# Optimization experiments

Hardware: AMD Instinct MI355X
Metric: run time of the kernel (lower is better)

## Reference

```python
import jax, jax.numpy as jnp
import numpy as np

EPS = 1e-6

def _rmsnorm(x, w):
    # normalize over last (head_dim) axis
    return x * jax.lax.rsqrt(jnp.mean(x * x, axis=-1, keepdims=True) + EPS) * w

def _rope(x, cos, sin):
    # x: [B, H, S, D]; cos/sin: [S, D]
    d = x.shape[-1]
    x1, x2 = x[..., : d // 2], x[..., d // 2 :]
    rot = jnp.concatenate([-x2, x1], axis=-1)
    return x * cos[None, None] + rot * sin[None, None]

def setup_inputs() -> dict:
    key = jax.random.key(0)
    B, S, D_MODEL = 1, 2048, 2048
    HEADS, HEAD_DIM, NKV = 32, 64, 8
    d_out = HEADS * HEAD_DIM
    kv_d_out = NKV * HEAD_DIM
    ks = jax.random.split(key, 8)
    x = jax.random.normal(ks[0], (B, S, D_MODEL), dtype=jnp.float32)
    # RoPE tables
    inv_freq = 1.0 / (10000.0 ** (jnp.arange(0, HEAD_DIM, 2, dtype=jnp.float32) / HEAD_DIM))
    pos = jnp.arange(S, dtype=jnp.float32)
    ang = pos[:, None] * inv_freq[None, :]            # [S, D/2]
    ang = jnp.concatenate([ang, ang], axis=-1)        # [S, D]
    sin, cos = jnp.sin(ang), jnp.cos(ang)
    mask = jnp.tril(jnp.ones((S, S), dtype=bool))     # causal: True = attend
    sd = 0.02
    Wq = jax.random.normal(ks[1], (D_MODEL, d_out), dtype=jnp.float32) * sd
    Wk = jax.random.normal(ks[2], (D_MODEL, kv_d_out), dtype=jnp.float32) * sd
    Wv = jax.random.normal(ks[3], (D_MODEL, kv_d_out), dtype=jnp.float32) * sd
    Wo = jax.random.normal(ks[4], (d_out, D_MODEL), dtype=jnp.float32) * sd
    bo = jnp.zeros((D_MODEL,), dtype=jnp.float32)
    q_scale = jnp.ones((HEAD_DIM,), dtype=jnp.float32)
    k_scale = jnp.ones((HEAD_DIM,), dtype=jnp.float32)
    return {"x": x, "sin": sin, "cos": cos, "mask": mask, "Wq": Wq, "Wk": Wk,
            "Wv": Wv, "Wo": Wo, "bo": bo, "q_scale": q_scale, "k_scale": k_scale}

def reference(x, sin, cos, mask, Wq, Wk, Wv, Wo, bo, q_scale, k_scale):
    B, S, _ = x.shape
    HEADS, HEAD_DIM, NKV = 32, 64, 8
    GS = HEADS // NKV  # group size = 4
    q = (x @ Wq).reshape(B, S, HEADS, HEAD_DIM).transpose(0, 2, 1, 3)  # [B,H,S,D]
    k = (x @ Wk).reshape(B, S, NKV, HEAD_DIM).transpose(0, 2, 1, 3)    # [B,G,S,D]
    v = (x @ Wv).reshape(B, S, NKV, HEAD_DIM).transpose(0, 2, 1, 3)    # [B,G,S,D]
    q = _rmsnorm(q, q_scale)
    k = _rmsnorm(k, k_scale)
    q = _rope(q, cos, sin)
    k = _rope(k, cos, sin)
    # GQA without materializing repeated k/v: group query heads per kv group
    qg = q.reshape(B, NKV, GS, S, HEAD_DIM)
    scale = 1.0 / jnp.sqrt(jnp.asarray(HEAD_DIM, dtype=x.dtype))
    scores = jnp.einsum('bghqd,bgkd->bghqk', qg, k) * scale  # [B,G,Gs,S,S]
    scores = jnp.where(mask[None, None, None], scores, jnp.asarray(-jnp.inf, dtype=scores.dtype))
    attn = jax.nn.softmax(scores, axis=-1)
    out = jnp.einsum('bghqk,bgkd->bghqd', attn, v)            # [B,G,Gs,S,D]
    out = out.reshape(B, HEADS, S, HEAD_DIM).transpose(0, 2, 1, 3).reshape(B, S, HEADS * HEAD_DIM)
    return out @ Wo + bo
```

## Files before the change

kernel.cpp:

```cpp
#include <hip/hip_runtime.h>
#include <stdint.h>


typedef __bf16 bf16x8 __attribute__((ext_vector_type(8)));
typedef __bf16 bf16x4v __attribute__((ext_vector_type(4)));
typedef float f32x4 __attribute__((ext_vector_type(4)));

#define MFMA_BF16(a, b, c) __builtin_amdgcn_mfma_f32_16x16x32_bf16(a, b, c, 0, 0, 0)

#if __has_builtin(__builtin_amdgcn_exp2f)
#define EXP2F(x) __builtin_amdgcn_exp2f(x)
#else
#define EXP2F(x) __expf((x) * 0.69314718055994531f)
#endif

#define QSCALE 0.18033688011112042f
#define SHIFT2 11.541560327111707f

__device__ __forceinline__ unsigned short f2bf(float f) {
  unsigned int u = __float_as_uint(f);
  u += 0x7fffu + ((u >> 16) & 1u);
  return (unsigned short)(u >> 16);
}
__device__ __forceinline__ float bf2f(unsigned short b) {
  return __uint_as_float(((unsigned int)b) << 16);
}

__device__ __forceinline__ void gload_lds16(const unsigned short* gsrc,
                                            unsigned short* ldst) {
  __builtin_amdgcn_global_load_lds(
      (const __attribute__((address_space(1))) unsigned int*)gsrc,
      (__attribute__((address_space(3))) unsigned int*)ldst, 16, 0, 0);
}

__global__ __launch_bounds__(256) void cvt_bf16(const float* __restrict__ X,
                                                unsigned short* __restrict__ Y, int n) {
  int i = (blockIdx.x * 256 + threadIdx.x) * 4;
  if (i < n) {
    float4 v = *(const float4*)&X[i];
    ushort4 o;
    o.x = f2bf(v.x); o.y = f2bf(v.y); o.z = f2bf(v.z); o.w = f2bf(v.w);
    *(ushort4*)&Y[i] = o;
  }
}

__global__ __launch_bounds__(256) void transpose_all(const float* __restrict__ Wq,
                                                     const float* __restrict__ Wk,
                                                     const float* __restrict__ Wv,
                                                     const float* __restrict__ Wo,
                                                     unsigned short* __restrict__ Wqkvt,
                                                     unsigned short* __restrict__ Wot) {
  int bx = blockIdx.x;
  const float* W;
  unsigned short* T;
  int N, nb;
  if (bx < 32)      { W = Wq; T = Wqkvt;                       N = 2048; nb = bx * 64; }
  else if (bx < 40) { W = Wk; T = Wqkvt + 2048 * 2048;         N = 512;  nb = (bx - 32) * 64; }
  else if (bx < 48) { W = Wv; T = Wqkvt + (size_t)2560 * 2048; N = 512;  nb = (bx - 40) * 64; }
  else              { W = Wo; T = Wot;                         N = 2048; nb = (bx - 48) * 64; }
  int kb = blockIdx.y * 64;
  int tid = threadIdx.x;
  __shared__ float tile[64][65];
#pragma unroll
  for (int i = 0; i < 16; i++) {
    int idx = tid + i * 256;
    int r = idx >> 6, c = idx & 63;
    tile[r][c] = W[(size_t)(kb + r) * N + nb + c];
  }
  __syncthreads();
#pragma unroll
  for (int i = 0; i < 8; i++) {
    int idx = tid + i * 256;
    int r = idx >> 5, cp = idx & 31;
    ushort2 o;
    o.x = f2bf(tile[2 * cp][r]);
    o.y = f2bf(tile[2 * cp + 1][r]);
    *(ushort2*)&T[(size_t)(nb + r) * 2048 + kb + 2 * cp] = o;
  }
}

#define GEMM_DBUF(A_, B_, m0_, n0_)                                            \
  int quad = lane >> 4, l16 = lane & 15;                                       \
  int wrow = (w & 1) * 32, wcol = (w >> 1) * 64;                               \
  int rsub = lane >> 3, csub = lane & 7;                                       \
  int chunk = csub ^ rsub;                                                     \
  int slotL = quad ^ (l16 & 7);                                                \
  const unsigned short* gA = &A_[(size_t)(m0_ + w * 16 + rsub) * 2048 + chunk * 8]; \
  const unsigned short* gB = &B_[(size_t)(n0_ + w * 32 + rsub) * 2048 + chunk * 8]; \
  int laOff = (w * 16) * 64 + lane * 8;                                        \
  int lbOff = 64 * 64 + (w * 32) * 64 + lane * 8;                              \
  f32x4 acc[2][4];                                                             \
  _Pragma("unroll") for (int i = 0; i < 2; i++)                                \
      _Pragma("unroll") for (int j = 0; j < 4; j++)                            \
          acc[i][j] = (f32x4){0.f, 0.f, 0.f, 0.f};                             \
  {                                                                            \
    unsigned short* sp = &Stage[0][0];                                         \
    gload_lds16(gA, sp + laOff);                                               \
    gload_lds16(gA + 8 * 2048, sp + laOff + 8 * 64);                           \
    gload_lds16(gB, sp + lbOff);                                               \
    gload_lds16(gB + 8 * 2048, sp + lbOff + 8 * 64);                           \
    gload_lds16(gB + 16 * 2048, sp + lbOff + 16 * 64);                         \
    gload_lds16(gB + 24 * 2048, sp + lbOff + 24 * 64);                         \
  }                                                                            \
  for (int k0 = 0; k0 < 2048; k0 += 64) {                                      \
    __syncthreads();                                                           \
    unsigned short* cur = &Stage[(k0 >> 6) & 1][0];                            \
    unsigned short* nxt = &Stage[((k0 >> 6) + 1) & 1][0];                      \
    if (k0 + 64 < 2048) {                                                      \
      int kn = k0 + 64;                                                        \
      gload_lds16(gA + kn, nxt + laOff);                                       \
      gload_lds16(gA + 8 * 2048 + kn, nxt + laOff + 8 * 64);                   \
      gload_lds16(gB + kn, nxt + lbOff);                                       \
      gload_lds16(gB + 8 * 2048 + kn, nxt + lbOff + 8 * 64);                   \
      gload_lds16(gB + 16 * 2048 + kn, nxt + lbOff + 16 * 64);                 \
      gload_lds16(gB + 24 * 2048 + kn, nxt + lbOff + 24 * 64);                 \
    }                                                                          \
    const unsigned short* As = cur;                                            \
    const unsigned short* Bs = cur + 64 * 64;                                  \
    bf16x8 af[2][2], bfr[4][2];                                                \
    _Pragma("unroll") for (int i = 0; i < 2; i++) {                            \
      int base = (wrow + i * 16 + l16) * 64;                                   \
      af[i][0] = *(const bf16x8*)&As[base + slotL * 8];                        \
      af[i][1] = *(const bf16x8*)&As[base + (slotL ^ 4) * 8];                  \
    }                                                                          \
    _Pragma("unroll") for (int j = 0; j < 4; j++) {                            \
      int base = (wcol + j * 16 + l16) * 64;                                   \
      bfr[j][0] = *(const bf16x8*)&Bs[base + slotL * 8];                       \
      bfr[j][1] = *(const bf16x8*)&Bs[base + (slotL ^ 4) * 8];                 \
    }                                                                          \
    _Pragma("unroll") for (int kc = 0; kc < 2; kc++)                           \
        _Pragma("unroll") for (int i = 0; i < 2; i++)                          \
            _Pragma("unroll") for (int j = 0; j < 4; j++)                      \
                acc[i][j] = MFMA_BF16(af[i][kc], bfr[j][kc], acc[i][j]);       \
  }

__global__ __launch_bounds__(256, 3) void gemm_qkv(const unsigned short* __restrict__ A,
                                                   const unsigned short* __restrict__ B,
                                                   const float* __restrict__ sinp,
                                                   const float* __restrict__ cosp,
                                                   const float* __restrict__ q_scale,
                                                   const float* __restrict__ k_scale,
                                                   unsigned short* __restrict__ qh,
                                                   unsigned short* __restrict__ kh,
                                                   unsigned short* __restrict__ vtmp) {
  __shared__ __align__(16) unsigned short Stage[2][192 * 64];
  int tid = threadIdx.x;
  int w = tid >> 6, lane = tid & 63;
  int m0 = blockIdx.y * 64;
  int n0 = blockIdx.x * 128;
  GEMM_DBUF(A, B, m0, n0)

  int hd = blockIdx.x * 2 + (w >> 1);
  if (hd < 40) {
    const float* scl = (hd < 32) ? q_scale : k_scale;
    float wsc[4];
#pragma unroll
    for (int j = 0; j < 4; j++) wsc[j] = scl[j * 16 + l16];
    float oscale = (hd < 32) ? QSCALE : 1.0f;
#pragma unroll
    for (int i = 0; i < 2; i++)
#pragma unroll
      for (int r = 0; r < 4; r++) {
        float ss = 0.f;
#pragma unroll
        for (int j = 0; j < 4; j++) ss += acc[i][j][r] * acc[i][j][r];
#pragma unroll
        for (int off = 8; off; off >>= 1) ss += __shfl_xor(ss, off);
        float inv = rsqrtf(ss * (1.f / 64.f) + 1e-6f);
        int s = m0 + wrow + i * 16 + quad * 4 + r;
        float xn[4];
#pragma unroll
        for (int j = 0; j < 4; j++) xn[j] = acc[i][j][r] * inv * wsc[j];
#pragma unroll
        for (int j = 0; j < 4; j++) {
          int d = j * 16 + l16;
          float rot = (j < 2) ? -xn[j + 2] : xn[j - 2];
          float out = (xn[j] * cosp[s * 64 + d] + rot * sinp[s * 64 + d]) * oscale;
          if (hd < 32) qh[(size_t)s * 2048 + hd * 64 + d] = f2bf(out);
          else         kh[(size_t)s * 512 + (hd - 32) * 64 + d] = f2bf(out);
        }
      }
  } else {
    int g = hd - 40;
#pragma unroll
    for (int i = 0; i < 2; i++)
#pragma unroll
      for (int r = 0; r < 4; r++) {
        int s = m0 + wrow + i * 16 + quad * 4 + r;
#pragma unroll
        for (int j = 0; j < 4; j++)
          vtmp[(size_t)s * 512 + g * 64 + j * 16 + l16] = f2bf(acc[i][j][r]);
      }
  }
}

__global__ __launch_bounds__(256, 3) void gemm_out(const unsigned short* __restrict__ A,
                                                   const unsigned short* __restrict__ B,
                                                   float* __restrict__ C,
                                                   const float* __restrict__ bias) {
  __shared__ __align__(16) unsigned short Stage[2][192 * 64];
  int tid = threadIdx.x;
  int w = tid >> 6, lane = tid & 63;
  int m0 = blockIdx.y * 64;
  int n0 = blockIdx.x * 128;
  GEMM_DBUF(A, B, m0, n0)

#pragma unroll
  for (int i = 0; i < 2; i++) {
    int row = m0 + wrow + i * 16 + quad * 4;
#pragma unroll
    for (int j = 0; j < 4; j++) {
      int col = n0 + wcol + j * 16 + l16;
      float b = bias[col];
#pragma unroll
      for (int r = 0; r < 4; r++)
        C[(size_t)(row + r) * 2048 + col] = acc[i][j][r] + b;
    }
  }
}

__global__ __launch_bounds__(256) void v_transpose(const unsigned short* __restrict__ vtmp,
                                                   unsigned short* __restrict__ vt) {
  __shared__ unsigned short tile[64][65];
  int s0 = blockIdx.x * 64;
  int g = blockIdx.y;
  int tid = threadIdx.x;
#pragma unroll
  for (int i = 0; i < 16; i++) {
    int idx = tid + i * 256;
    int r = idx >> 6, c = idx & 63;
    tile[r][c] = vtmp[(size_t)(s0 + r) * 512 + g * 64 + c];
  }
  __syncthreads();
#pragma unroll
  for (int i = 0; i < 16; i++) {
    int idx = tid + i * 256;
    int d = idx >> 6, slot = idx & 63;
    int qd = (slot >> 3) & 3, c = slot >> 5, j = slot & 7;
    int key = 16 * ((j >> 2) * 2 + c) + qd * 4 + (j & 3);
    vt[(size_t)(g * 64 + d) * 2048 + s0 + slot] = tile[key][d];
  }
}

__global__ __launch_bounds__(256, 4) void attention(const unsigned short* __restrict__ qh,
                                                    const unsigned short* __restrict__ kh,
                                                    const unsigned short* __restrict__ vt,
                                                    unsigned short* __restrict__ Opart,
                                                    float* __restrict__ Lpart) {
  int h = blockIdx.y;
  int g = h >> 2;
  int z = blockIdx.z;
  int tile = (blockIdx.x + blockIdx.y) & 31;
  int q0 = tile * 64;
  int w = threadIdx.x >> 6;
  int lane = threadIdx.x & 63;
  int quad = lane >> 4;
  int l16 = lane & 15;
  int qrow0 = q0 + w * 16;

  __shared__ __align__(16) unsigned short Stage[8192];
  unsigned short* Ks = Stage;
  unsigned short* Vs = Stage + 4096;

  int rsub = lane >> 3;
  int csub = lane & 7;
  int chunk = csub ^ rsub;

  const unsigned short* kg = &kh[(size_t)(w * 16 + rsub) * 512 + g * 64 + chunk * 8];
  const unsigned short* vg = &vt[(size_t)(g * 64 + w * 16 + rsub) * 2048 + chunk * 8];
  unsigned short* kl = Ks + (w * 16) * 64 + lane * 8;
  unsigned short* vl = Vs + (w * 16) * 64 + lane * 8;

  int posL = quad ^ (l16 & 7);
  int fL = l16 * 64 + posL * 8;
  int fH = l16 * 64 + (posL ^ 4) * 8;

  bf16x8 bq0 = *(const bf16x8*)&qh[(size_t)(qrow0 + l16) * 2048 + h * 64 + quad * 8];
  bf16x8 bq1 = *(const bf16x8*)&qh[(size_t)(qrow0 + l16) * 2048 + h * 64 + 32 + quad * 8];

  f32x4 o[4];
#pragma unroll
  for (int j = 0; j < 4; j++) o[j] = (f32x4){0.f, 0.f, 0.f, 0.f};
  float l_run = 0.f;

  int T = tile + 1;
  int it0 = z ? (T >> 1) : 0;
  int it1 = z ? T : (T >> 1);
  for (int it = it0; it < it1; ++it) {
    int n0 = it << 6;
    __syncthreads();
    gload_lds16(kg + (size_t)n0 * 512, kl);
    gload_lds16(kg + (size_t)(n0 + 8) * 512, kl + 8 * 64);
    gload_lds16(vg + n0, vl);
    gload_lds16(vg + n0 + 8 * 2048, vl + 8 * 64);
    __syncthreads();

    f32x4 s[4];
#pragma unroll
    for (int t = 0; t < 4; ++t) {
      bf16x8 kfl = *(const bf16x8*)&Ks[t * 1024 + fL];
      bf16x8 kfh = *(const bf16x8*)&Ks[t * 1024 + fH];
      f32x4 zz = (f32x4){0.f, 0.f, 0.f, 0.f};
      zz = MFMA_BF16(kfl, bq0, zz);
      s[t] = MFMA_BF16(kfh, bq1, zz);
    }

    float pv[4][4];
    if (it == T - 1) {
      int qg = qrow0 + l16;
#pragma unroll
      for (int t = 0; t < 4; ++t)
#pragma unroll
        for (int r = 0; r < 4; ++r) {
          int key = n0 + t * 16 + quad * 4 + r;
          float p = (key <= qg) ? EXP2F(s[t][r] - SHIFT2) : 0.f;
          l_run += p;
          pv[t][r] = p;
        }
    } else {
#pragma unroll
      for (int t = 0; t < 4; ++t)
#pragma unroll
        for (int r = 0; r < 4; ++r) {
          float p = EXP2F(s[t][r] - SHIFT2);
          l_run += p;
          pv[t][r] = p;
        }
    }

    bf16x8 pf0, pf1;
#pragma unroll
    for (int j = 0; j < 4; ++j) {
      pf0[j] = (__bf16)pv[0][j];
      pf0[j + 4] = (__bf16)pv[2][j];
      pf1[j] = (__bf16)pv[1][j];
      pf1[j + 4] = (__bf16)pv[3][j];
    }

#pragma unroll
    for (int jd = 0; jd < 4; ++jd) {
      bf16x8 vfl = *(const bf16x8*)&Vs[jd * 1024 + fL];
      bf16x8 vfh = *(const bf16x8*)&Vs[jd * 1024 + fH];
      o[jd] = MFMA_BF16(vfl, pf0, o[jd]);
      o[jd] = MFMA_BF16(vfh, pf1, o[jd]);
    }
  }

  l_run += __shfl_xor(l_run, 16);
  l_run += __shfl_xor(l_run, 32);
  if (lane < 16)
    Lpart[(size_t)z * 65536 + (qrow0 + l16) * 32 + h] = l_run;

  __syncthreads();
  unsigned short* Ob = Stage + w * (16 * 68);
#pragma unroll
  for (int jd = 0; jd < 4; ++jd) {
    bf16x4v pk;
#pragma unroll
    for (int r = 0; r < 4; ++r) pk[r] = (__bf16)o[jd][r];
    *(bf16x4v*)&Ob[l16 * 68 + jd * 16 + quad * 4] = pk;
  }
  __threadfence_block();
#pragma unroll
  for (int rr = 0; rr < 2; ++rr) {
    int cidx = rr * 64 + lane;
    int row = cidx >> 3, ch = cidx & 7;
    bf16x8 v = *(const bf16x8*)&Ob[row * 68 + ch * 8];
    *(bf16x8*)&Opart[((size_t)z * 2048 + qrow0 + row) * 2048 + h * 64 + ch * 8] = v;
  }
}

__global__ __launch_bounds__(256) void combine(const unsigned short* __restrict__ Opart,
                                               const float* __restrict__ Lpart,
                                               unsigned short* __restrict__ aout) {
  int idx = blockIdx.x * 256 + threadIdx.x;
  int s = idx >> 9;
  int col = (idx & 511) * 4;
  int h = col >> 6;
  float l = Lpart[s * 32 + h] + Lpart[65536 + s * 32 + h];
  float linv = 1.f / l;
  ushort4 a = *(const ushort4*)&Opart[(size_t)s * 2048 + col];
  ushort4 b = *(const ushort4*)&Opart[(size_t)(2048 + s) * 2048 + col];
  ushort4 o;
  o.x = f2bf((bf2f(a.x) + bf2f(b.x)) * linv);
  o.y = f2bf((bf2f(a.y) + bf2f(b.y)) * linv);
  o.z = f2bf((bf2f(a.z) + bf2f(b.z)) * linv);
  o.w = f2bf((bf2f(a.w) + bf2f(b.w)) * linv);
  *(ushort4*)&aout[(size_t)s * 2048 + col] = o;
}

extern "C" void kernel_launch(void* const* d_in, const int* in_sizes, int n_in,
                              void* d_out, int out_size, void* d_ws, size_t ws_size,
                              hipStream_t stream) {
  (void)in_sizes; (void)n_in; (void)out_size; (void)ws_size;
  const float* x    = (const float*)d_in[0];
  const float* sinp = (const float*)d_in[1];
  const float* cosp = (const float*)d_in[2];
  const float* Wq = (const float*)d_in[4];
  const float* Wk = (const float*)d_in[5];
  const float* Wv = (const float*)d_in[6];
  const float* Wo = (const float*)d_in[7];
  const float* bo = (const float*)d_in[8];
  const float* q_scale = (const float*)d_in[9];
  const float* k_scale = (const float*)d_in[10];
  float* outp = (float*)d_out;

  uint8_t* ws = (uint8_t*)d_ws;
  const size_t MB = 1024 * 1024;
  unsigned short* xb    = (unsigned short*)(ws);
  unsigned short* Wqkvt = (unsigned short*)(ws + 8 * MB);
  unsigned short* Wot   = (unsigned short*)(ws + 20 * MB);
  unsigned short* qh    = (unsigned short*)(ws + 28 * MB);
  unsigned short* kh    = (unsigned short*)(ws + 36 * MB);
  unsigned short* vtmp  = (unsigned short*)(ws + 38 * MB);
  unsigned short* vt    = (unsigned short*)(ws + 40 * MB);
  unsigned short* aout  = (unsigned short*)(ws + 42 * MB);
  unsigned short* Opart = (unsigned short*)(ws + 50 * MB);
  float*          Lpart = (float*)(ws + 66 * MB);

  cvt_bf16<<<4096, 256, 0, stream>>>(x, xb, 2048 * 2048);
  transpose_all<<<dim3(80, 32), 256, 0, stream>>>(Wq, Wk, Wv, Wo, Wqkvt, Wot);
  gemm_qkv<<<dim3(24, 32), 256, 0, stream>>>(xb, Wqkvt, sinp, cosp, q_scale, k_scale,
                                             qh, kh, vtmp);
  v_transpose<<<dim3(32, 8), 256, 0, stream>>>(vtmp, vt);
  attention<<<dim3(32, 32, 2), 256, 0, stream>>>(qh, kh, vt, Opart, Lpart);
  combine<<<4096, 256, 0, stream>>>(Opart, Lpart, aout);
  gemm_out<<<dim3(16, 32), 256, 0, stream>>>(aout, Wot, outp, bo);
}
```

Before: 222.9 us.

## Fuse x conversion, V transpose and split-K combine into neighbouring kernels

Folds the x fp32-to-bf16 conversion into the weight-transpose launch as extra blocks, writes V straight into the permuted transposed layout from the QKV GEMM epilogue, and drops the two-way split of attention over keys along with its combine kernel. Each attention block now normalizes by 1/l itself and writes bf16 output directly. This cuts launch count and the intermediate global traffic for vtmp, Opart and Lpart. The cost is half as many attention blocks with causal-imbalanced work, so long-tail tiles lose parallelism.

```diff
diff --git a/kernel.cpp b/kernel.cpp
--- a/kernel.cpp
+++ b/kernel.cpp
@@ -22,9 +22,6 @@
   u += 0x7fffu + ((u >> 16) & 1u);
   return (unsigned short)(u >> 16);
 }
-__device__ __forceinline__ float bf2f(unsigned short b) {
-  return __uint_as_float(((unsigned int)b) << 16);
-}
 
 __device__ __forceinline__ void gload_lds16(const unsigned short* gsrc,
                                             unsigned short* ldst) {
@@ -33,24 +30,28 @@
       (__attribute__((address_space(3))) unsigned int*)ldst, 16, 0, 0);
 }
 
-__global__ __launch_bounds__(256) void cvt_bf16(const float* __restrict__ X,
-                                                unsigned short* __restrict__ Y, int n) {
-  int i = (blockIdx.x * 256 + threadIdx.x) * 4;
-  if (i < n) {
-    float4 v = *(const float4*)&X[i];
-    ushort4 o;
-    o.x = f2bf(v.x); o.y = f2bf(v.y); o.z = f2bf(v.z); o.w = f2bf(v.w);
-    *(ushort4*)&Y[i] = o;
-  }
-}
-
 __global__ __launch_bounds__(256) void transpose_all(const float* __restrict__ Wq,
                                                      const float* __restrict__ Wk,
                                                      const float* __restrict__ Wv,
                                                      const float* __restrict__ Wo,
+                                                     const float* __restrict__ x,
                                                      unsigned short* __restrict__ Wqkvt,
-                                                     unsigned short* __restrict__ Wot) {
+                                                     unsigned short* __restrict__ Wot,
+                                                     unsigned short* __restrict__ xb) {
   int bx = blockIdx.x;
+  int tid = threadIdx.x;
+  if (bx >= 80) {
+    int bid = (bx - 80) * 32 + blockIdx.y;
+#pragma unroll
+    for (int p = 0; p < 8; p++) {
+      int i = bid * 8192 + p * 1024 + tid * 4;
+      float4 v = *(const float4*)&x[i];
+      ushort4 o;
+      o.x = f2bf(v.x); o.y = f2bf(v.y); o.z = f2bf(v.z); o.w = f2bf(v.w);
+      *(ushort4*)&xb[i] = o;
+    }
+    return;
+  }
   const float* W;
   unsigned short* T;
   int N, nb;
@@ -59,7 +60,6 @@
   else if (bx < 48) { W = Wv; T = Wqkvt + (size_t)2560 * 2048; N = 512;  nb = (bx - 40) * 64; }
   else              { W = Wo; T = Wot;                         N = 2048; nb = (bx - 48) * 64; }
   int kb = blockIdx.y * 64;
-  int tid = threadIdx.x;
   __shared__ float tile[64][65];
 #pragma unroll
   for (int i = 0; i < 16; i++) {
@@ -142,7 +142,7 @@
                                                    const float* __restrict__ k_scale,
                                                    unsigned short* __restrict__ qh,
                                                    unsigned short* __restrict__ kh,
-                                                   unsigned short* __restrict__ vtmp) {
+                                                   unsigned short* __restrict__ vt) {
   __shared__ __align__(16) unsigned short Stage[2][192 * 64];
   int tid = threadIdx.x;
   int w = tid >> 6, lane = tid & 63;
@@ -183,14 +183,17 @@
   } else {
     int g = hd - 40;
 #pragma unroll
-    for (int i = 0; i < 2; i++)
-#pragma unroll
-      for (int r = 0; r < 4; r++) {
-        int s = m0 + wrow + i * 16 + quad * 4 + r;
-#pragma unroll
-        for (int j = 0; j < 4; j++)
-          vtmp[(size_t)s * 512 + g * 64 + j * 16 + l16] = f2bf(acc[i][j][r]);
+    for (int i = 0; i < 2; i++) {
+      int t = (wrow + i * 16) >> 4;
+      int slotb = (t & 1) * 32 + quad * 8 + (t >> 1) * 4;
+#pragma unroll
+      for (int j = 0; j < 4; j++) {
+        bf16x4v pk;
+#pragma unroll
+        for (int r = 0; r < 4; r++) pk[r] = (__bf16)acc[i][j][r];
+        *(bf16x4v*)&vt[(size_t)(g * 64 + j * 16 + l16) * 2048 + m0 + slotb] = pk;
       }
+    }
   }
 }
 
@@ -219,37 +222,12 @@
   }
 }
 
-__global__ __launch_bounds__(256) void v_transpose(const unsigned short* __restrict__ vtmp,
-                                                   unsigned short* __restrict__ vt) {
-  __shared__ unsigned short tile[64][65];
-  int s0 = blockIdx.x * 64;
-  int g = blockIdx.y;
-  int tid = threadIdx.x;
-#pragma unroll
-  for (int i = 0; i < 16; i++) {
-    int idx = tid + i * 256;
-    int r = idx >> 6, c = idx & 63;
-    tile[r][c] = vtmp[(size_t)(s0 + r) * 512 + g * 64 + c];
-  }
-  __syncthreads();
-#pragma unroll
-  for (int i = 0; i < 16; i++) {
-    int idx = tid + i * 256;
-    int d = idx >> 6, slot = idx & 63;
-    int qd = (slot >> 3) & 3, c = slot >> 5, j = slot & 7;
-    int key = 16 * ((j >> 2) * 2 + c) + qd * 4 + (j & 3);
-    vt[(size_t)(g * 64 + d) * 2048 + s0 + slot] = tile[key][d];
-  }
-}
-
 __global__ __launch_bounds__(256, 4) void attention(const unsigned short* __restrict__ qh,
                                                     const unsigned short* __restrict__ kh,
                                                     const unsigned short* __restrict__ vt,
-                                                    unsigned short* __restrict__ Opart,
-                                                    float* __restrict__ Lpart) {
+                                                    unsigned short* __restrict__ aout) {
   int h = blockIdx.y;
   int g = h >> 2;
-  int z = blockIdx.z;
   int tile = (blockIdx.x + blockIdx.y) & 31;
   int q0 = tile * 64;
   int w = threadIdx.x >> 6;
@@ -284,9 +262,7 @@
   float l_run = 0.f;
 
   int T = tile + 1;
-  int it0 = z ? (T >> 1) : 0;
-  int it1 = z ? T : (T >> 1);
-  for (int it = it0; it < it1; ++it) {
+  for (int it = 0; it < T; ++it) {
     int n0 = it << 6;
     __syncthreads();
     gload_lds16(kg + (size_t)n0 * 512, kl);
@@ -348,8 +324,7 @@
 
   l_run += __shfl_xor(l_run, 16);
   l_run += __shfl_xor(l_run, 32);
-  if (lane < 16)
-    Lpart[(size_t)z * 65536 + (qrow0 + l16) * 32 + h] = l_run;
+  float linv = 1.f / l_run;
 
   __syncthreads();
   unsigned short* Ob = Stage + w * (16 * 68);
@@ -357,7 +332,7 @@
   for (int jd = 0; jd < 4; ++jd) {
     bf16x4v pk;
 #pragma unroll
-    for (int r = 0; r < 4; ++r) pk[r] = (__bf16)o[jd][r];
+    for (int r = 0; r < 4; ++r) pk[r] = (__bf16)(o[jd][r] * linv);
     *(bf16x4v*)&Ob[l16 * 68 + jd * 16 + quad * 4] = pk;
   }
   __threadfence_block();
@@ -366,27 +341,8 @@
     int cidx = rr * 64 + lane;
     int row = cidx >> 3, ch = cidx & 7;
     bf16x8 v = *(const bf16x8*)&Ob[row * 68 + ch * 8];
-    *(bf16x8*)&Opart[((size_t)z * 2048 + qrow0 + row) * 2048 + h * 64 + ch * 8] = v;
-  }
-}
-
-__global__ __launch_bounds__(256) void combine(const unsigned short* __restrict__ Opart,
-                                               const float* __restrict__ Lpart,
-                                               unsigned short* __restrict__ aout) {
-  int idx = blockIdx.x * 256 + threadIdx.x;
-  int s = idx >> 9;
-  int col = (idx & 511) * 4;
-  int h = col >> 6;
-  float l = Lpart[s * 32 + h] + Lpart[65536 + s * 32 + h];
-  float linv = 1.f / l;
-  ushort4 a = *(const ushort4*)&Opart[(size_t)s * 2048 + col];
-  ushort4 b = *(const ushort4*)&Opart[(size_t)(2048 + s) * 2048 + col];
-  ushort4 o;
-  o.x = f2bf((bf2f(a.x) + bf2f(b.x)) * linv);
-  o.y = f2bf((bf2f(a.y) + bf2f(b.y)) * linv);
-  o.z = f2bf((bf2f(a.z) + bf2f(b.z)) * linv);
-  o.w = f2bf((bf2f(a.w) + bf2f(b.w)) * linv);
-  *(ushort4*)&aout[(size_t)s * 2048 + col] = o;
+    *(bf16x8*)&aout[(size_t)(qrow0 + row) * 2048 + h * 64 + ch * 8] = v;
+  }
 }
 
 extern "C" void kernel_launch(void* const* d_in, const int* in_sizes, int n_in,
@@ -412,18 +368,12 @@
   unsigned short* Wot   = (unsigned short*)(ws + 20 * MB);
   unsigned short* qh    = (unsigned short*)(ws + 28 * MB);
   unsigned short* kh    = (unsigned short*)(ws + 36 * MB);
-  unsigned short* vtmp  = (unsigned short*)(ws + 38 * MB);
-  unsigned short* vt    = (unsigned short*)(ws + 40 * MB);
-  unsigned short* aout  = (unsigned short*)(ws + 42 * MB);
-  unsigned short* Opart = (unsigned short*)(ws + 50 * MB);
-  float*          Lpart = (float*)(ws + 66 * MB);
-
-  cvt_bf16<<<4096, 256, 0, stream>>>(x, xb, 2048 * 2048);
-  transpose_all<<<dim3(80, 32), 256, 0, stream>>>(Wq, Wk, Wv, Wo, Wqkvt, Wot);
+  unsigned short* vt    = (unsigned short*)(ws + 38 * MB);
+  unsigned short* aout  = (unsigned short*)(ws + 40 * MB);
+
+  transpose_all<<<dim3(96, 32), 256, 0, stream>>>(Wq, Wk, Wv, Wo, x, Wqkvt, Wot, xb);
   gemm_qkv<<<dim3(24, 32), 256, 0, stream>>>(xb, Wqkvt, sinp, cosp, q_scale, k_scale,
-                                             qh, kh, vtmp);
-  v_transpose<<<dim3(32, 8), 256, 0, stream>>>(vtmp, vt);
-  attention<<<dim3(32, 32, 2), 256, 0, stream>>>(qh, kh, vt, Opart, Lpart);
-  combine<<<4096, 256, 0, stream>>>(Opart, Lpart, aout);
+                                             qh, kh, vt);
+  attention<<<dim3(32, 32), 256, 0, stream>>>(qh, kh, vt, aout);
   gemm_out<<<dim3(16, 32), 256, 0, stream>>>(aout, Wot, outp, bo);
 }
```

New measurement: 213.1 us. 1.05x faster.
